# Performance work log

Hardware: AMD Instinct MI355X
Metric: run time of the kernel (lower is better)

Reference implementation:

```python
import jax, jax.numpy as jnp
import numpy as np

DT = 0.01
NJ = 7
GRAV = 9.81
Q_LOWER = jnp.array([-2.9671, -1.8326, -2.9671, -3.1416, -2.9671, -0.0873, -2.9671], jnp.float32)
Q_UPPER = jnp.array([ 2.9671,  1.8326,  2.9671,  0.0,     2.9671,  3.8223,  2.9671], jnp.float32)


def _skew(v):
    z = jnp.zeros((), v.dtype)
    return jnp.stack([jnp.stack([z, -v[2], v[1]]),
                      jnp.stack([v[2], z, -v[0]]),
                      jnp.stack([-v[1], v[0], z])])


def _mot_X(E, r):
    # 6x6 spatial motion transform [[E,0],[-E*skew(r),E]]
    zero = jnp.zeros_like(E)
    top = jnp.concatenate([E, zero], axis=1)
    bot = jnp.concatenate([-E @ _skew(r), E], axis=1)
    return jnp.concatenate([top, bot], axis=0)


def _crm(v):
    # spatial motion cross-product matrix for v=[w;v0]
    Sw, Sv = _skew(v[:3]), _skew(v[3:])
    zero = jnp.zeros_like(Sw)
    top = jnp.concatenate([Sw, zero], axis=1)
    bot = jnp.concatenate([Sv, Sw], axis=1)
    return jnp.concatenate([top, bot], axis=0)


def _step_single(x, u, axes, R_tree, p_tree, I_sp):
    dt_ = x.dtype
    q = jnp.clip(x[:NJ], Q_LOWER.astype(dt_), Q_UPPER.astype(dt_))
    qd = x[NJ:]
    # forward kinematics: per-joint 6x6 child<-parent transforms and motion subspaces
    Xups, Ss = [], []
    eye3 = jnp.eye(3, dtype=dt_)
    for i in range(NJ):
        a = axes[i]
        c, s = jnp.cos(q[i]), jnp.sin(q[i])
        R = c * eye3 + s * _skew(a) + (1.0 - c) * jnp.outer(a, a)  # rodrigues
        Xj = _mot_X(R.T, jnp.zeros(3, dt_))
        Xt = _mot_X(R_tree[i], p_tree[i])
        Xups.append(Xj @ Xt)
        Ss.append(jnp.concatenate([a, jnp.zeros(3, dt_)]))
    # RNEA bias force h (qdd=0, gravity, zero base velocity, identity base pose)
    v_prev = jnp.zeros(6, dt_)
    a_prev = jnp.array([0.0, 0.0, 0.0, 0.0, 0.0, GRAV], dt_)  # a_base = -g trick
    fs = []
    for i in range(NJ):
        vJ = Ss[i] * qd[i]
        v = Xups[i] @ v_prev + vJ
        acc = Xups[i] @ a_prev + _crm(v) @ vJ
        Iv = I_sp[i] @ v
        f = I_sp[i] @ acc - _crm(v).T @ Iv  # crf(v) = -crm(v)^T
        fs.append(f)
        v_prev, a_prev = v, acc
    h = [None] * NJ
    for i in range(NJ - 1, -1, -1):
        h[i] = Ss[i] @ fs[i]
        if i > 0:
            fs[i - 1] = fs[i - 1] + Xups[i].T @ fs[i]
    h = jnp.stack(h)
    # CRBA mass matrix (serial chain, parent(i)=i-1)
    Ic = [I_sp[i] for i in range(NJ)]
    M = jnp.zeros((NJ, NJ), dt_)
    for i in range(NJ - 1, -1, -1):
        if i > 0:
            Ic[i - 1] = Ic[i - 1] + Xups[i].T @ Ic[i] @ Xups[i]
        F = Ic[i] @ Ss[i]
        M = M.at[i, i].set(Ss[i] @ F)
        for j in range(i - 1, -1, -1):
            F = Xups[j + 1].T @ F
            mij = Ss[j] @ F
            M = M.at[i, j].set(mij).at[j, i].set(mij)
    M = M + 1e-8 * jnp.eye(NJ, dtype=dt_)
    qdd = jnp.linalg.solve(M, (u - h)[:, None])[:, 0]
    qd_new = qd + DT * qdd
    q_new = q + DT * qd_new
    return jnp.concatenate([q_new, qd_new])


def setup_inputs() -> dict:
    B = 65536
    key = jax.random.key(0)
    k1, k2 = jax.random.split(key)
    x = jax.random.normal(k1, (B, 14), jnp.float32)
    u = jax.random.normal(k2, (B, 7), jnp.float32)
    rng = np.random.default_rng(0)
    # unit joint axes
    axes = rng.normal(size=(NJ, 3))
    axes = axes / np.linalg.norm(axes, axis=1, keepdims=True)
    # orthonormal fixed parent->child rotations (det +1)
    R_tree = np.empty((NJ, 3, 3))
    for i in range(NJ):
        Q, _ = np.linalg.qr(rng.normal(size=(3, 3)))
        if np.linalg.det(Q) < 0:
            Q[:, 0] = -Q[:, 0]
        R_tree[i] = Q
    p_tree = 0.2 * rng.normal(size=(NJ, 3))
    # SPD 6x6 spatial inertias: [[Ibar, m*Cx],[m*Cx^T, m*I3]]
    I_sp = np.empty((NJ, 6, 6))
    for i in range(NJ):
        m = float(rng.uniform(1.0, 5.0))
        c = 0.05 * rng.normal(size=3)
        Cx = np.array([[0, -c[2], c[1]], [c[2], 0, -c[0]], [-c[1], c[0], 0]])
        A = 0.1 * rng.normal(size=(3, 3))
        Ic_ = A @ A.T + 0.05 * np.eye(3)
        Ibar = Ic_ + m * Cx @ Cx.T
        I_sp[i] = np.block([[Ibar, m * Cx], [m * Cx.T, m * np.eye(3)]])
    return {
        "x": x, "u": u,
        "axes": jnp.asarray(axes, jnp.float32),
        "R_tree": jnp.asarray(R_tree, jnp.float32),
        "p_tree": jnp.asarray(p_tree, jnp.float32),
        "I_sp": jnp.asarray(I_sp, jnp.float32),
    }


def reference(x, u, axes, R_tree, p_tree, I_sp):
    return jax.vmap(_step_single, in_axes=(0, 0, None, None, None, None))(
        x, u, axes, R_tree, p_tree, I_sp)
```

## Files before the change

### kernel.cpp

```cpp
#include <hip/hip_runtime.h>
#include <math.h>

#define NJ 7
#define DTF 0.01f
#define GRAVF 9.81f
#define MIX(i,j) ((i)*((i)+1)/2 + (j))
#define MPAD 29
#define CW 28


__device__ __forceinline__ void cross3(const float* a, const float* b, float* o){
    o[0] = a[1]*b[2] - a[2]*b[1];
    o[1] = a[2]*b[0] - a[0]*b[2];
    o[2] = a[0]*b[1] - a[1]*b[0];
}
__device__ __forceinline__ void mv3(const float* E, const float* x, float* y){
    y[0] = E[0]*x[0] + E[1]*x[1] + E[2]*x[2];
    y[1] = E[3]*x[0] + E[4]*x[1] + E[5]*x[2];
    y[2] = E[6]*x[0] + E[7]*x[1] + E[8]*x[2];
}
__device__ __forceinline__ void mtv3(const float* E, const float* x, float* y){
    y[0] = E[0]*x[0] + E[3]*x[1] + E[6]*x[2];
    y[1] = E[1]*x[0] + E[4]*x[1] + E[7]*x[2];
    y[2] = E[2]*x[0] + E[5]*x[1] + E[8]*x[2];
}
__device__ __forceinline__ void symv(const float* S, const float* x, float* y){
    y[0] = S[0]*x[0] + S[1]*x[1] + S[2]*x[2];
    y[1] = S[1]*x[0] + S[3]*x[1] + S[4]*x[2];
    y[2] = S[2]*x[0] + S[4]*x[1] + S[5]*x[2];
}
__device__ __forceinline__ void mm3(const float* A, const float* B, float* o){
#pragma unroll
    for (int r = 0; r < 3; r++)
#pragma unroll
        for (int c = 0; c < 3; c++)
            o[r*3+c] = A[r*3]*B[c] + A[r*3+1]*B[3+c] + A[r*3+2]*B[6+c];
}
__device__ __forceinline__ void congr(const float* E, const float* X, float* o){
    float t[9];
#pragma unroll
    for (int r = 0; r < 3; r++)
#pragma unroll
        for (int c = 0; c < 3; c++)
            t[r*3+c] = E[r]*X[c] + E[3+r]*X[3+c] + E[6+r]*X[6+c];
    mm3(t, E, o);
}
__device__ __forceinline__ void makeE(const float* a, const float* Rt, float s, float c, float* E){
    float omc = 1.0f - c;
    float RT[9];
    RT[0] = c + omc*a[0]*a[0];       RT[1] =  s*a[2] + omc*a[0]*a[1]; RT[2] = -s*a[1] + omc*a[0]*a[2];
    RT[3] = -s*a[2] + omc*a[1]*a[0]; RT[4] = c + omc*a[1]*a[1];       RT[5] =  s*a[0] + omc*a[1]*a[2];
    RT[6] =  s*a[1] + omc*a[2]*a[0]; RT[7] = -s*a[0] + omc*a[2]*a[1]; RT[8] = c + omc*a[2]*a[2];
    mm3(RT, Rt, E);
}
__device__ __forceinline__ void loadJ(const float* __restrict__ cst, int i,
                                      float* Rt, float* a, float* p,
                                      float* SA, float* h, float& m){
    const float4* cb4 = (const float4*)(cst + i*CW);
    float4 c0=cb4[0], c1=cb4[1], c2=cb4[2], c3=cb4[3], c4=cb4[4], c5=cb4[5], c6=cb4[6];
    Rt[0]=c0.x; Rt[1]=c0.y; Rt[2]=c0.z; Rt[3]=c0.w;
    Rt[4]=c1.x; Rt[5]=c1.y; Rt[6]=c1.z; Rt[7]=c1.w;
    Rt[8]=c2.x; a[0]=c2.y; a[1]=c2.z; a[2]=c2.w;
    p[0]=c3.x; p[1]=c3.y; p[2]=c3.z;
    SA[0]=c4.x; SA[1]=c4.y; SA[2]=c4.z; SA[3]=c4.w;
    SA[4]=c5.x; SA[5]=c5.y; h[0]=c5.z; h[1]=c5.w;
    h[2]=c6.x; m=c6.y;
}
__device__ __forceinline__ void loadI(const float* __restrict__ cst, int i,
                                      float* SA, float* h, float& m){
    const float4* cb4 = (const float4*)(cst + i*CW);
    float4 c4=cb4[4], c5=cb4[5], c6=cb4[6];
    SA[0]=c4.x; SA[1]=c4.y; SA[2]=c4.z; SA[3]=c4.w;
    SA[4]=c5.x; SA[5]=c5.y; h[0]=c5.z; h[1]=c5.w;
    h[2]=c6.x; m=c6.y;
}
__device__ __forceinline__ void loadAP(const float* __restrict__ cst, int i,
                                       float* a, float* p){
    const float4* cb4 = (const float4*)(cst + i*CW);
    float4 c2=cb4[2], c3=cb4[3];
    a[0]=c2.y; a[1]=c2.z; a[2]=c2.w;
    p[0]=c3.x; p[1]=c3.y; p[2]=c3.z;
}

__global__ void panda_prep(const float* __restrict__ g_ax, const float* __restrict__ g_Rt,
                           const float* __restrict__ g_pt, const float* __restrict__ g_I,
                           float* __restrict__ cst)
{
    int i = threadIdx.x;
    if (i >= NJ) return;
    float* o = cst + i*CW;
#pragma unroll
    for (int k = 0; k < 9; k++) o[k] = g_Rt[i*9+k];
    o[9]=g_ax[i*3]; o[10]=g_ax[i*3+1]; o[11]=g_ax[i*3+2];
    o[12]=g_pt[i*3]; o[13]=g_pt[i*3+1]; o[14]=g_pt[i*3+2]; o[15]=0.f;
    const float* I6 = g_I + i*36;
    o[16]=I6[0];  o[17]=I6[1];  o[18]=I6[2];
    o[19]=I6[7];  o[20]=I6[8];  o[21]=I6[14];
    o[22]=I6[16]; o[23]=I6[5];  o[24]=I6[9];
    o[25]=I6[21]; o[26]=0.f; o[27]=0.f;
}

__global__ __launch_bounds__(128)
void panda_step(const float* __restrict__ x, const float* __restrict__ u,
                const float* __restrict__ cst, float* __restrict__ out, int B)
{
    __shared__ float s_M[64*MPAD];

    const int role = threadIdx.x >> 6;
    const int lane = threadIdx.x & 63;
    const int e    = blockIdx.x*64 + lane;
    const bool act = (e < B);

    const float QL[NJ] = {-2.9671f,-1.8326f,-2.9671f,-3.1416f,-2.9671f,-0.0873f,-2.9671f};
    const float QU[NJ] = { 2.9671f, 1.8326f, 2.9671f, 0.0f,    2.9671f, 3.8223f, 2.9671f};

    float q[NJ], qd[NJ], sn[NJ], cs[NJ];
    if (act){
        float xl[14];
        const float2* x2 = (const float2*)(x + e*14);
#pragma unroll
        for (int i = 0; i < 7; i++){ float2 v = x2[i]; xl[2*i] = v.x; xl[2*i+1] = v.y; }
#pragma unroll
        for (int i = 0; i < NJ; i++){
            q[i]  = fminf(fmaxf(xl[i], QL[i]), QU[i]);
            qd[i] = xl[NJ + i];
            __sincosf(q[i], &sn[i], &cs[i]);
        }
    }

    float rhs[NJ];

    if (act && role == 1){
        float SA[6], hc[3], mc;
        {
            float dm; loadI(cst, 6, SA, hc, dm); mc = dm;
        }
        float Fk[NJ][6];
        float Mx[28];
#pragma unroll
        for (int i = NJ-1; i >= 0; i--){
            float Rt[9], a[3], p[3], SAn[6], hn[3], mn;
            loadJ(cst, i, Rt, a, p, SAn, hn, mn);
            float SAm[6], hm[3], mm_;
            if (i > 0) loadI(cst, i-1, SAm, hm, mm_);
            symv(SA, a, &Fk[i][0]);
            Fk[i][3] = a[1]*hc[2] - a[2]*hc[1];
            Fk[i][4] = a[2]*hc[0] - a[0]*hc[2];
            Fk[i][5] = a[0]*hc[1] - a[1]*hc[0];
#pragma unroll
            for (int k = i; k < NJ; k++)
                Mx[MIX(k,i)] = a[0]*Fk[k][0] + a[1]*Fk[k][1] + a[2]*Fk[k][2];
            if (i > 0){
                float E[9]; makeE(a, Rt, sn[i], cs[i], E);
                float Af[9] = {SA[0],SA[1],SA[2], SA[1],SA[3],SA[4], SA[2],SA[4],SA[5]};
                float Ap[9]; congr(E, Af, Ap);
                float hr[3]; mtv3(E, hc, hr);
                float hpd = hr[0]*p[0]+hr[1]*p[1]+hr[2]*p[2];
                float ppd = p[0]*p[0]+p[1]*p[1]+p[2]*p[2];
                float dga = 2.0f*hpd + mc*ppd;
                SA[0] = Ap[0] - 2.0f*p[0]*hr[0] - mc*p[0]*p[0] + dga + SAm[0];
                SA[1] = Ap[1] - p[0]*hr[1] - hr[0]*p[1] - mc*p[0]*p[1] + SAm[1];
                SA[2] = Ap[2] - p[0]*hr[2] - hr[0]*p[2] - mc*p[0]*p[2] + SAm[2];
                SA[3] = Ap[4] - 2.0f*p[1]*hr[1] - mc*p[1]*p[1] + dga + SAm[3];
                SA[4] = Ap[5] - p[1]*hr[2] - hr[1]*p[2] - mc*p[1]*p[2] + SAm[4];
                SA[5] = Ap[8] - 2.0f*p[2]*hr[2] - mc*p[2]*p[2] + dga + SAm[5];
                hc[0] = hr[0] + mc*p[0] + hm[0];
                hc[1] = hr[1] + mc*p[1] + hm[1];
                hc[2] = hr[2] + mc*p[2] + hm[2];
                mc += mm_;
#pragma unroll
                for (int k = i; k < NJ; k++){
                    float tm[3], tf[3], cp[3];
                    mtv3(E, &Fk[k][0], tm); mtv3(E, &Fk[k][3], tf);
                    cross3(p, tf, cp);
                    Fk[k][0]=tm[0]+cp[0]; Fk[k][1]=tm[1]+cp[1]; Fk[k][2]=tm[2]+cp[2];
                    Fk[k][3]=tf[0];       Fk[k][4]=tf[1];       Fk[k][5]=tf[2];
                }
            }
        }
#pragma unroll
        for (int i = 0; i < NJ; i++) Mx[MIX(i,i)] += 1e-8f;
#pragma unroll
        for (int k = 0; k < NJ; k++){
            float d = Mx[MIX(k,k)];
#pragma unroll
            for (int j = 0; j < NJ; j++) if (j < k) d -= Mx[MIX(k,j)]*Mx[MIX(k,j)];
            float linv = __builtin_amdgcn_rsqf(d);
            Mx[MIX(k,k)] = linv;
#pragma unroll
            for (int i2 = k+1; i2 < NJ; i2++){
                float s2 = Mx[MIX(i2,k)];
#pragma unroll
                for (int j = 0; j < NJ; j++) if (j < k) s2 -= Mx[MIX(i2,j)]*Mx[MIX(k,j)];
                Mx[MIX(i2,k)] = s2 * linv;
            }
        }
#pragma unroll
        for (int j = 0; j < 28; j++) s_M[lane*MPAD + j] = Mx[j];
    }
    else if (act){
#pragma unroll
        for (int i = 0; i < NJ; i++) rhs[i] = u[e*NJ + i];
        float Earr[NJ][9];
        float FF[NJ][6];
        float w[3]  = {0.f,0.f,0.f}, vl[3] = {0.f,0.f,0.f};
        float aw[3] = {0.f,0.f,0.f}, av[3] = {0.f,0.f,GRAVF};
#pragma unroll
        for (int i = 0; i < NJ; i++){
            float Rt[9], a[3], p[3], SAi[6], hi[3], mi;
            loadJ(cst, i, Rt, a, p, SAi, hi, mi);
            float* E = &Earr[i][0];
            makeE(a, Rt, sn[i], cs[i], E);
            float qdi = qd[i];
            float tw[3]; mv3(E, w, tw);
            float nw[3] = { tw[0]+a[0]*qdi, tw[1]+a[1]*qdi, tw[2]+a[2]*qdi };
            float cwp[3]; cross3(w, p, cwp);
            float t1[3] = { vl[0]+cwp[0], vl[1]+cwp[1], vl[2]+cwp[2] };
            float nvl[3]; mv3(E, t1, nvl);
            float taw[3]; mv3(E, aw, taw);
            float cna[3]; cross3(nw, a, cna);
            float naw[3] = { taw[0]+qdi*cna[0], taw[1]+qdi*cna[1], taw[2]+qdi*cna[2] };
            float cap[3]; cross3(aw, p, cap);
            float t2[3] = { av[0]+cap[0], av[1]+cap[1], av[2]+cap[2] };
            float tav[3]; mv3(E, t2, tav);
            float cva[3]; cross3(nvl, a, cva);
            float nav[3] = { tav[0]+qdi*cva[0], tav[1]+qdi*cva[1], tav[2]+qdi*cva[2] };
            float Ivt[3], Iat[3], hxv[3], hxa[3];
            symv(SAi, nw, Ivt);  cross3(hi, nvl, hxv);
            symv(SAi, naw, Iat); cross3(hi, nav, hxa);
#pragma unroll
            for (int k = 0; k < 3; k++){ Ivt[k] += hxv[k]; Iat[k] += hxa[k]; }
            float hxw[3], hxaw[3];
            cross3(hi, nw, hxw); cross3(hi, naw, hxaw);
            float Ivb[3] = { mi*nvl[0]-hxw[0], mi*nvl[1]-hxw[1], mi*nvl[2]-hxw[2] };
            float Iab[3] = { mi*nav[0]-hxaw[0], mi*nav[1]-hxaw[1], mi*nav[2]-hxaw[2] };
            float c1[3], c2[3], c3[3];
            cross3(nw, Ivt, c1); cross3(nvl, Ivb, c2); cross3(nw, Ivb, c3);
            FF[i][0] = Iat[0]+c1[0]+c2[0];
            FF[i][1] = Iat[1]+c1[1]+c2[1];
            FF[i][2] = Iat[2]+c1[2]+c2[2];
            FF[i][3] = Iab[0]+c3[0];
            FF[i][4] = Iab[1]+c3[1];
            FF[i][5] = Iab[2]+c3[2];
#pragma unroll
            for (int k = 0; k < 3; k++){ w[k]=nw[k]; vl[k]=nvl[k]; aw[k]=naw[k]; av[k]=nav[k]; }
        }
#pragma unroll
        for (int i = NJ-1; i >= 0; i--){
            float a[3], p[3];
            loadAP(cst, i, a, p);
            rhs[i] -= a[0]*FF[i][0] + a[1]*FF[i][1] + a[2]*FF[i][2];
            if (i > 0){
                const float* E = &Earr[i][0];
                float tm[3], tf[3], cp[3];
                mtv3(E, &FF[i][0], tm); mtv3(E, &FF[i][3], tf);
                cross3(p, tf, cp);
                FF[i-1][0]+=tm[0]+cp[0]; FF[i-1][1]+=tm[1]+cp[1]; FF[i-1][2]+=tm[2]+cp[2];
                FF[i-1][3]+=tf[0];       FF[i-1][4]+=tf[1];       FF[i-1][5]+=tf[2];
            }
        }
    }

    __syncthreads();

    if (act && role == 0){
        float Mx[28];
#pragma unroll
        for (int j = 0; j < 28; j++) Mx[j] = s_M[lane*MPAD + j];
        float y[NJ];
#pragma unroll
        for (int i = 0; i < NJ; i++){
            float s2 = rhs[i];
#pragma unroll
            for (int j = 0; j < NJ; j++) if (j < i) s2 -= Mx[MIX(i,j)]*y[j];
            y[i] = s2 * Mx[MIX(i,i)];
        }
        float z[NJ];
#pragma unroll
        for (int i = NJ-1; i >= 0; i--){
            float s2 = y[i];
#pragma unroll
            for (int j = NJ-1; j >= 0; j--) if (j > i) s2 -= Mx[MIX(j,i)]*z[j];
            z[i] = s2 * Mx[MIX(i,i)];
        }
        float o14[14];
#pragma unroll
        for (int i = 0; i < NJ; i++){
            float qdn = qd[i] + DTF*z[i];
            o14[i]      = q[i] + DTF*qdn;
            o14[NJ + i] = qdn;
        }
        float2* o2 = (float2*)(out + e*14);
#pragma unroll
        for (int i = 0; i < 7; i++){ float2 v; v.x = o14[2*i]; v.y = o14[2*i+1]; o2[i] = v; }
    }
}

extern "C" void kernel_launch(void* const* d_in, const int* in_sizes, int n_in,
                              void* d_out, int out_size, void* d_ws, size_t ws_size,
                              hipStream_t stream) {
    const float* x   = (const float*)d_in[0];
    const float* u   = (const float*)d_in[1];
    const float* ax  = (const float*)d_in[2];
    const float* Rt  = (const float*)d_in[3];
    const float* pt  = (const float*)d_in[4];
    const float* Isp = (const float*)d_in[5];
    float* out = (float*)d_out;
    float* cst = (float*)d_ws;
    int B = in_sizes[0] / 14;
    hipLaunchKernelGGL(panda_prep, dim3(1), dim3(64), 0, stream, ax, Rt, pt, Isp, cst);
    int grid = (B + 63) / 64;
    hipLaunchKernelGGL(panda_step, dim3(grid), dim3(128), 0, stream,
                       x, u, cst, out, B);
}
```

Baseline: 78.42 us.

## Split warp-specialized kernel into separate CRBA and RNEA+solve kernels via global workspace

Replaces the single kernel, where one wavefront computed the CRBA mass matrix and Cholesky factor while another computed the RNEA bias, with two kernels. The first writes each item's Cholesky factor to a global workspace, and the second reads it back after RNEA to do the solve. This removes the shared-memory handoff and the __syncthreads, and lets each kernel use 256-thread blocks with lower register pressure. The cost is an extra kernel launch and 112 bytes per item of global write and read. Joint limits also move to constant memory.

```diff
diff --git a/kernel.cpp b/kernel.cpp
--- a/kernel.cpp
+++ b/kernel.cpp
@@ -5,8 +5,8 @@
 #define DTF 0.01f
 #define GRAVF 9.81f
 #define MIX(i,j) ((i)*((i)+1)/2 + (j))
-#define MPAD 29
 #define CW 28
+#define LOFF 256
 
 
 __device__ __forceinline__ void cross3(const float* a, const float* b, float* o){
@@ -82,6 +82,9 @@
     p[0]=c3.x; p[1]=c3.y; p[2]=c3.z;
 }
 
+__constant__ float QL_c[NJ] = {-2.9671f,-1.8326f,-2.9671f,-3.1416f,-2.9671f,-0.0873f,-2.9671f};
+__constant__ float QU_c[NJ] = { 2.9671f, 1.8326f, 2.9671f, 0.0f,    2.9671f, 3.8223f, 2.9671f};
+
 __global__ void panda_prep(const float* __restrict__ g_ax, const float* __restrict__ g_Rt,
                            const float* __restrict__ g_pt, const float* __restrict__ g_I,
                            float* __restrict__ cst)
@@ -100,200 +103,216 @@
     o[25]=I6[21]; o[26]=0.f; o[27]=0.f;
 }
 
-__global__ __launch_bounds__(128)
-void panda_step(const float* __restrict__ x, const float* __restrict__ u,
-                const float* __restrict__ cst, float* __restrict__ out, int B)
+__global__ __launch_bounds__(256)
+void panda_crba(const float* __restrict__ x, const float* __restrict__ cst,
+                float* __restrict__ Lw, int B)
 {
-    __shared__ float s_M[64*MPAD];
-
-    const int role = threadIdx.x >> 6;
-    const int lane = threadIdx.x & 63;
-    const int e    = blockIdx.x*64 + lane;
-    const bool act = (e < B);
-
-    const float QL[NJ] = {-2.9671f,-1.8326f,-2.9671f,-3.1416f,-2.9671f,-0.0873f,-2.9671f};
-    const float QU[NJ] = { 2.9671f, 1.8326f, 2.9671f, 0.0f,    2.9671f, 3.8223f, 2.9671f};
+    int e = blockIdx.x*blockDim.x + threadIdx.x;
+    if (e >= B) return;
+
+    float sn[NJ], cs[NJ];
+    {
+        const float2* x2 = (const float2*)(x + e*14);
+        float q8[8];
+#pragma unroll
+        for (int i = 0; i < 4; i++){ float2 v = x2[i]; q8[2*i] = v.x; q8[2*i+1] = v.y; }
+#pragma unroll
+        for (int i = 0; i < NJ; i++){
+            float qi = fminf(fmaxf(q8[i], QL_c[i]), QU_c[i]);
+            __sincosf(qi, &sn[i], &cs[i]);
+        }
+    }
+
+    float SA[6], hc[3], mc;
+    { float dm; loadI(cst, 6, SA, hc, dm); mc = dm; }
+    float Fk[NJ][6];
+    float Mx[28];
+#pragma unroll
+    for (int i = NJ-1; i >= 0; i--){
+        float Rt[9], a[3], p[3], SAo[6], ho[3], mo;
+        loadJ(cst, i, Rt, a, p, SAo, ho, mo);
+        float SAm[6], hm[3], mm_;
+        if (i > 0) loadI(cst, i-1, SAm, hm, mm_);
+        symv(SA, a, &Fk[i][0]);
+        Fk[i][3] = a[1]*hc[2] - a[2]*hc[1];
+        Fk[i][4] = a[2]*hc[0] - a[0]*hc[2];
+        Fk[i][5] = a[0]*hc[1] - a[1]*hc[0];
+#pragma unroll
+        for (int k = i; k < NJ; k++)
+            Mx[MIX(k,i)] = a[0]*Fk[k][0] + a[1]*Fk[k][1] + a[2]*Fk[k][2];
+        if (i > 0){
+            float E[9]; makeE(a, Rt, sn[i], cs[i], E);
+            float Af[9] = {SA[0],SA[1],SA[2], SA[1],SA[3],SA[4], SA[2],SA[4],SA[5]};
+            float Ap[9]; congr(E, Af, Ap);
+            float hr[3]; mtv3(E, hc, hr);
+            float hpd = hr[0]*p[0]+hr[1]*p[1]+hr[2]*p[2];
+            float ppd = p[0]*p[0]+p[1]*p[1]+p[2]*p[2];
+            float dga = 2.0f*hpd + mc*ppd;
+            SA[0] = Ap[0] - 2.0f*p[0]*hr[0] - mc*p[0]*p[0] + dga + SAm[0];
+            SA[1] = Ap[1] - p[0]*hr[1] - hr[0]*p[1] - mc*p[0]*p[1] + SAm[1];
+            SA[2] = Ap[2] - p[0]*hr[2] - hr[0]*p[2] - mc*p[0]*p[2] + SAm[2];
+            SA[3] = Ap[4] - 2.0f*p[1]*hr[1] - mc*p[1]*p[1] + dga + SAm[3];
+            SA[4] = Ap[5] - p[1]*hr[2] - hr[1]*p[2] - mc*p[1]*p[2] + SAm[4];
+            SA[5] = Ap[8] - 2.0f*p[2]*hr[2] - mc*p[2]*p[2] + dga + SAm[5];
+            hc[0] = hr[0] + mc*p[0] + hm[0];
+            hc[1] = hr[1] + mc*p[1] + hm[1];
+            hc[2] = hr[2] + mc*p[2] + hm[2];
+            mc += mm_;
+#pragma unroll
+            for (int k = i; k < NJ; k++){
+                float tm[3], tf[3], cp[3];
+                mtv3(E, &Fk[k][0], tm); mtv3(E, &Fk[k][3], tf);
+                cross3(p, tf, cp);
+                Fk[k][0]=tm[0]+cp[0]; Fk[k][1]=tm[1]+cp[1]; Fk[k][2]=tm[2]+cp[2];
+                Fk[k][3]=tf[0];       Fk[k][4]=tf[1];       Fk[k][5]=tf[2];
+            }
+        }
+    }
+#pragma unroll
+    for (int i = 0; i < NJ; i++) Mx[MIX(i,i)] += 1e-8f;
+#pragma unroll
+    for (int k = 0; k < NJ; k++){
+        float d = Mx[MIX(k,k)];
+#pragma unroll
+        for (int j = 0; j < NJ; j++) if (j < k) d -= Mx[MIX(k,j)]*Mx[MIX(k,j)];
+        float linv = __builtin_amdgcn_rsqf(d);
+        Mx[MIX(k,k)] = linv;
+#pragma unroll
+        for (int i2 = k+1; i2 < NJ; i2++){
+            float s2 = Mx[MIX(i2,k)];
+#pragma unroll
+            for (int j = 0; j < NJ; j++) if (j < k) s2 -= Mx[MIX(i2,j)]*Mx[MIX(k,j)];
+            Mx[MIX(i2,k)] = s2 * linv;
+        }
+    }
+    float4* Lo = (float4*)(Lw + e*28);
+#pragma unroll
+    for (int g = 0; g < 7; g++){
+        float4 v; v.x = Mx[4*g]; v.y = Mx[4*g+1]; v.z = Mx[4*g+2]; v.w = Mx[4*g+3];
+        Lo[g] = v;
+    }
+}
+
+__global__ __launch_bounds__(256)
+void panda_rnea_solve(const float* __restrict__ x, const float* __restrict__ u,
+                      const float* __restrict__ cst, const float* __restrict__ Lw,
+                      float* __restrict__ out, int B)
+{
+    int e = blockIdx.x*blockDim.x + threadIdx.x;
+    if (e >= B) return;
 
     float q[NJ], qd[NJ], sn[NJ], cs[NJ];
-    if (act){
+    {
         float xl[14];
         const float2* x2 = (const float2*)(x + e*14);
 #pragma unroll
         for (int i = 0; i < 7; i++){ float2 v = x2[i]; xl[2*i] = v.x; xl[2*i+1] = v.y; }
 #pragma unroll
         for (int i = 0; i < NJ; i++){
-            q[i]  = fminf(fmaxf(xl[i], QL[i]), QU[i]);
+            q[i]  = fminf(fmaxf(xl[i], QL_c[i]), QU_c[i]);
             qd[i] = xl[NJ + i];
             __sincosf(q[i], &sn[i], &cs[i]);
         }
     }
-
     float rhs[NJ];
-
-    if (act && role == 1){
-        float SA[6], hc[3], mc;
-        {
-            float dm; loadI(cst, 6, SA, hc, dm); mc = dm;
-        }
-        float Fk[NJ][6];
-        float Mx[28];
-#pragma unroll
-        for (int i = NJ-1; i >= 0; i--){
-            float Rt[9], a[3], p[3], SAn[6], hn[3], mn;
-            loadJ(cst, i, Rt, a, p, SAn, hn, mn);
-            float SAm[6], hm[3], mm_;
-            if (i > 0) loadI(cst, i-1, SAm, hm, mm_);
-            symv(SA, a, &Fk[i][0]);
-            Fk[i][3] = a[1]*hc[2] - a[2]*hc[1];
-            Fk[i][4] = a[2]*hc[0] - a[0]*hc[2];
-            Fk[i][5] = a[0]*hc[1] - a[1]*hc[0];
-#pragma unroll
-            for (int k = i; k < NJ; k++)
-                Mx[MIX(k,i)] = a[0]*Fk[k][0] + a[1]*Fk[k][1] + a[2]*Fk[k][2];
-            if (i > 0){
-                float E[9]; makeE(a, Rt, sn[i], cs[i], E);
-                float Af[9] = {SA[0],SA[1],SA[2], SA[1],SA[3],SA[4], SA[2],SA[4],SA[5]};
-                float Ap[9]; congr(E, Af, Ap);
-                float hr[3]; mtv3(E, hc, hr);
-                float hpd = hr[0]*p[0]+hr[1]*p[1]+hr[2]*p[2];
-                float ppd = p[0]*p[0]+p[1]*p[1]+p[2]*p[2];
-                float dga = 2.0f*hpd + mc*ppd;
-                SA[0] = Ap[0] - 2.0f*p[0]*hr[0] - mc*p[0]*p[0] + dga + SAm[0];
-                SA[1] = Ap[1] - p[0]*hr[1] - hr[0]*p[1] - mc*p[0]*p[1] + SAm[1];
-                SA[2] = Ap[2] - p[0]*hr[2] - hr[0]*p[2] - mc*p[0]*p[2] + SAm[2];
-                SA[3] = Ap[4] - 2.0f*p[1]*hr[1] - mc*p[1]*p[1] + dga + SAm[3];
-                SA[4] = Ap[5] - p[1]*hr[2] - hr[1]*p[2] - mc*p[1]*p[2] + SAm[4];
-                SA[5] = Ap[8] - 2.0f*p[2]*hr[2] - mc*p[2]*p[2] + dga + SAm[5];
-                hc[0] = hr[0] + mc*p[0] + hm[0];
-                hc[1] = hr[1] + mc*p[1] + hm[1];
-                hc[2] = hr[2] + mc*p[2] + hm[2];
-                mc += mm_;
-#pragma unroll
-                for (int k = i; k < NJ; k++){
-                    float tm[3], tf[3], cp[3];
-                    mtv3(E, &Fk[k][0], tm); mtv3(E, &Fk[k][3], tf);
-                    cross3(p, tf, cp);
-                    Fk[k][0]=tm[0]+cp[0]; Fk[k][1]=tm[1]+cp[1]; Fk[k][2]=tm[2]+cp[2];
-                    Fk[k][3]=tf[0];       Fk[k][4]=tf[1];       Fk[k][5]=tf[2];
-                }
-            }
-        }
-#pragma unroll
-        for (int i = 0; i < NJ; i++) Mx[MIX(i,i)] += 1e-8f;
-#pragma unroll
-        for (int k = 0; k < NJ; k++){
-            float d = Mx[MIX(k,k)];
-#pragma unroll
-            for (int j = 0; j < NJ; j++) if (j < k) d -= Mx[MIX(k,j)]*Mx[MIX(k,j)];
-            float linv = __builtin_amdgcn_rsqf(d);
-            Mx[MIX(k,k)] = linv;
-#pragma unroll
-            for (int i2 = k+1; i2 < NJ; i2++){
-                float s2 = Mx[MIX(i2,k)];
-#pragma unroll
-                for (int j = 0; j < NJ; j++) if (j < k) s2 -= Mx[MIX(i2,j)]*Mx[MIX(k,j)];
-                Mx[MIX(i2,k)] = s2 * linv;
-            }
-        }
-#pragma unroll
-        for (int j = 0; j < 28; j++) s_M[lane*MPAD + j] = Mx[j];
-    }
-    else if (act){
-#pragma unroll
-        for (int i = 0; i < NJ; i++) rhs[i] = u[e*NJ + i];
-        float Earr[NJ][9];
-        float FF[NJ][6];
-        float w[3]  = {0.f,0.f,0.f}, vl[3] = {0.f,0.f,0.f};
-        float aw[3] = {0.f,0.f,0.f}, av[3] = {0.f,0.f,GRAVF};
-#pragma unroll
-        for (int i = 0; i < NJ; i++){
-            float Rt[9], a[3], p[3], SAi[6], hi[3], mi;
-            loadJ(cst, i, Rt, a, p, SAi, hi, mi);
-            float* E = &Earr[i][0];
-            makeE(a, Rt, sn[i], cs[i], E);
-            float qdi = qd[i];
-            float tw[3]; mv3(E, w, tw);
-            float nw[3] = { tw[0]+a[0]*qdi, tw[1]+a[1]*qdi, tw[2]+a[2]*qdi };
-            float cwp[3]; cross3(w, p, cwp);
-            float t1[3] = { vl[0]+cwp[0], vl[1]+cwp[1], vl[2]+cwp[2] };
-            float nvl[3]; mv3(E, t1, nvl);
-            float taw[3]; mv3(E, aw, taw);
-            float cna[3]; cross3(nw, a, cna);
-            float naw[3] = { taw[0]+qdi*cna[0], taw[1]+qdi*cna[1], taw[2]+qdi*cna[2] };
-            float cap[3]; cross3(aw, p, cap);
-            float t2[3] = { av[0]+cap[0], av[1]+cap[1], av[2]+cap[2] };
-            float tav[3]; mv3(E, t2, tav);
-            float cva[3]; cross3(nvl, a, cva);
-            float nav[3] = { tav[0]+qdi*cva[0], tav[1]+qdi*cva[1], tav[2]+qdi*cva[2] };
-            float Ivt[3], Iat[3], hxv[3], hxa[3];
-            symv(SAi, nw, Ivt);  cross3(hi, nvl, hxv);
-            symv(SAi, naw, Iat); cross3(hi, nav, hxa);
-#pragma unroll
-            for (int k = 0; k < 3; k++){ Ivt[k] += hxv[k]; Iat[k] += hxa[k]; }
-            float hxw[3], hxaw[3];
-            cross3(hi, nw, hxw); cross3(hi, naw, hxaw);
-            float Ivb[3] = { mi*nvl[0]-hxw[0], mi*nvl[1]-hxw[1], mi*nvl[2]-hxw[2] };
-            float Iab[3] = { mi*nav[0]-hxaw[0], mi*nav[1]-hxaw[1], mi*nav[2]-hxaw[2] };
-            float c1[3], c2[3], c3[3];
-            cross3(nw, Ivt, c1); cross3(nvl, Ivb, c2); cross3(nw, Ivb, c3);
-            FF[i][0] = Iat[0]+c1[0]+c2[0];
-            FF[i][1] = Iat[1]+c1[1]+c2[1];
-            FF[i][2] = Iat[2]+c1[2]+c2[2];
-            FF[i][3] = Iab[0]+c3[0];
-            FF[i][4] = Iab[1]+c3[1];
-            FF[i][5] = Iab[2]+c3[2];
-#pragma unroll
-            for (int k = 0; k < 3; k++){ w[k]=nw[k]; vl[k]=nvl[k]; aw[k]=naw[k]; av[k]=nav[k]; }
-        }
-#pragma unroll
-        for (int i = NJ-1; i >= 0; i--){
-            float a[3], p[3];
-            loadAP(cst, i, a, p);
-            rhs[i] -= a[0]*FF[i][0] + a[1]*FF[i][1] + a[2]*FF[i][2];
-            if (i > 0){
-                const float* E = &Earr[i][0];
-                float tm[3], tf[3], cp[3];
-                mtv3(E, &FF[i][0], tm); mtv3(E, &FF[i][3], tf);
-                cross3(p, tf, cp);
-                FF[i-1][0]+=tm[0]+cp[0]; FF[i-1][1]+=tm[1]+cp[1]; FF[i-1][2]+=tm[2]+cp[2];
-                FF[i-1][3]+=tf[0];       FF[i-1][4]+=tf[1];       FF[i-1][5]+=tf[2];
-            }
-        }
-    }
-
-    __syncthreads();
-
-    if (act && role == 0){
-        float Mx[28];
-#pragma unroll
-        for (int j = 0; j < 28; j++) Mx[j] = s_M[lane*MPAD + j];
-        float y[NJ];
-#pragma unroll
-        for (int i = 0; i < NJ; i++){
-            float s2 = rhs[i];
-#pragma unroll
-            for (int j = 0; j < NJ; j++) if (j < i) s2 -= Mx[MIX(i,j)]*y[j];
-            y[i] = s2 * Mx[MIX(i,i)];
-        }
-        float z[NJ];
-#pragma unroll
-        for (int i = NJ-1; i >= 0; i--){
-            float s2 = y[i];
-#pragma unroll
-            for (int j = NJ-1; j >= 0; j--) if (j > i) s2 -= Mx[MIX(j,i)]*z[j];
-            z[i] = s2 * Mx[MIX(i,i)];
-        }
-        float o14[14];
-#pragma unroll
-        for (int i = 0; i < NJ; i++){
-            float qdn = qd[i] + DTF*z[i];
-            o14[i]      = q[i] + DTF*qdn;
-            o14[NJ + i] = qdn;
-        }
-        float2* o2 = (float2*)(out + e*14);
-#pragma unroll
-        for (int i = 0; i < 7; i++){ float2 v; v.x = o14[2*i]; v.y = o14[2*i+1]; o2[i] = v; }
-    }
+#pragma unroll
+    for (int i = 0; i < NJ; i++) rhs[i] = u[e*NJ + i];
+
+    float Earr[NJ][9];
+    float FF[NJ][6];
+    float w[3]  = {0.f,0.f,0.f}, vl[3] = {0.f,0.f,0.f};
+    float aw[3] = {0.f,0.f,0.f}, av[3] = {0.f,0.f,GRAVF};
+#pragma unroll
+    for (int i = 0; i < NJ; i++){
+        float Rt[9], a[3], p[3], SAi[6], hi[3], mi;
+        loadJ(cst, i, Rt, a, p, SAi, hi, mi);
+        float* E = &Earr[i][0];
+        makeE(a, Rt, sn[i], cs[i], E);
+        float qdi = qd[i];
+        float tw[3]; mv3(E, w, tw);
+        float nw[3] = { tw[0]+a[0]*qdi, tw[1]+a[1]*qdi, tw[2]+a[2]*qdi };
+        float cwp[3]; cross3(w, p, cwp);
+        float t1[3] = { vl[0]+cwp[0], vl[1]+cwp[1], vl[2]+cwp[2] };
+        float nvl[3]; mv3(E, t1, nvl);
+        float taw[3]; mv3(E, aw, taw);
+        float cna[3]; cross3(nw, a, cna);
+        float naw[3] = { taw[0]+qdi*cna[0], taw[1]+qdi*cna[1], taw[2]+qdi*cna[2] };
+        float cap[3]; cross3(aw, p, cap);
+        float t2[3] = { av[0]+cap[0], av[1]+cap[1], av[2]+cap[2] };
+        float tav[3]; mv3(E, t2, tav);
+        float cva[3]; cross3(nvl, a, cva);
+        float nav[3] = { tav[0]+qdi*cva[0], tav[1]+qdi*cva[1], tav[2]+qdi*cva[2] };
+        float Ivt[3], Iat[3], hxv[3], hxa[3];
+        symv(SAi, nw, Ivt);  cross3(hi, nvl, hxv);
+        symv(SAi, naw, Iat); cross3(hi, nav, hxa);
+#pragma unroll
+        for (int k = 0; k < 3; k++){ Ivt[k] += hxv[k]; Iat[k] += hxa[k]; }
+        float hxw[3], hxaw[3];
+        cross3(hi, nw, hxw); cross3(hi, naw, hxaw);
+        float Ivb[3] = { mi*nvl[0]-hxw[0], mi*nvl[1]-hxw[1], mi*nvl[2]-hxw[2] };
+        float Iab[3] = { mi*nav[0]-hxaw[0], mi*nav[1]-hxaw[1], mi*nav[2]-hxaw[2] };
+        float c1[3], c2[3], c3[3];
+        cross3(nw, Ivt, c1); cross3(nvl, Ivb, c2); cross3(nw, Ivb, c3);
+        FF[i][0] = Iat[0]+c1[0]+c2[0];
+        FF[i][1] = Iat[1]+c1[1]+c2[1];
+        FF[i][2] = Iat[2]+c1[2]+c2[2];
+        FF[i][3] = Iab[0]+c3[0];
+        FF[i][4] = Iab[1]+c3[1];
+        FF[i][5] = Iab[2]+c3[2];
+#pragma unroll
+        for (int k = 0; k < 3; k++){ w[k]=nw[k]; vl[k]=nvl[k]; aw[k]=naw[k]; av[k]=nav[k]; }
+    }
+#pragma unroll
+    for (int i = NJ-1; i >= 0; i--){
+        float a[3], p[3];
+        loadAP(cst, i, a, p);
+        rhs[i] -= a[0]*FF[i][0] + a[1]*FF[i][1] + a[2]*FF[i][2];
+        if (i > 0){
+            const float* E = &Earr[i][0];
+            float tm[3], tf[3], cp[3];
+            mtv3(E, &FF[i][0], tm); mtv3(E, &FF[i][3], tf);
+            cross3(p, tf, cp);
+            FF[i-1][0]+=tm[0]+cp[0]; FF[i-1][1]+=tm[1]+cp[1]; FF[i-1][2]+=tm[2]+cp[2];
+            FF[i-1][3]+=tf[0];       FF[i-1][4]+=tf[1];       FF[i-1][5]+=tf[2];
+        }
+    }
+
+    float Mx[28];
+    {
+        const float4* Li = (const float4*)(Lw + e*28);
+#pragma unroll
+        for (int g = 0; g < 7; g++){
+            float4 v = Li[g];
+            Mx[4*g] = v.x; Mx[4*g+1] = v.y; Mx[4*g+2] = v.z; Mx[4*g+3] = v.w;
+        }
+    }
+    float y[NJ];
+#pragma unroll
+    for (int i = 0; i < NJ; i++){
+        float s2 = rhs[i];
+#pragma unroll
+        for (int j = 0; j < NJ; j++) if (j < i) s2 -= Mx[MIX(i,j)]*y[j];
+        y[i] = s2 * Mx[MIX(i,i)];
+    }
+    float z[NJ];
+#pragma unroll
+    for (int i = NJ-1; i >= 0; i--){
+        float s2 = y[i];
+#pragma unroll
+        for (int j = NJ-1; j >= 0; j--) if (j > i) s2 -= Mx[MIX(j,i)]*z[j];
+        z[i] = s2 * Mx[MIX(i,i)];
+    }
+
+    float o14[14];
+#pragma unroll
+    for (int i = 0; i < NJ; i++){
+        float qdn = qd[i] + DTF*z[i];
+        o14[i]      = q[i] + DTF*qdn;
+        o14[NJ + i] = qdn;
+    }
+    float2* o2 = (float2*)(out + e*14);
+#pragma unroll
+    for (int i = 0; i < 7; i++){ float2 v; v.x = o14[2*i]; v.y = o14[2*i+1]; o2[i] = v; }
 }
 
 extern "C" void kernel_launch(void* const* d_in, const int* in_sizes, int n_in,
@@ -307,9 +326,10 @@
     const float* Isp = (const float*)d_in[5];
     float* out = (float*)d_out;
     float* cst = (float*)d_ws;
+    float* Lw  = (float*)d_ws + LOFF;
     int B = in_sizes[0] / 14;
     hipLaunchKernelGGL(panda_prep, dim3(1), dim3(64), 0, stream, ax, Rt, pt, Isp, cst);
-    int grid = (B + 63) / 64;
-    hipLaunchKernelGGL(panda_step, dim3(grid), dim3(128), 0, stream,
-                       x, u, cst, out, B);
-}
+    int grid = (B + 255) / 256;
+    hipLaunchKernelGGL(panda_crba, dim3(grid), dim3(256), 0, stream, x, cst, Lw, B);
+    hipLaunchKernelGGL(panda_rnea_solve, dim3(grid), dim3(256), 0, stream, x, u, cst, Lw, out, B);
+}
```

Measured after the change: 84.63 us. 7.9% more time.
